# Kernel optimization log

Hardware: AMD Instinct MI355X
Metric: run time of the kernel (lower is better)

Reference implementation:

```python
import jax, jax.numpy as jnp
import numpy as np

EPS = 1e-5  # BatchNorm eps (torch default)

def _bn(x, gamma, beta):
    # training-mode BatchNorm over the edge/node (leading) axis, biased var
    mean = x.mean(axis=0, keepdims=True)
    var = x.var(axis=0, keepdims=True)
    return (x - mean) * jax.lax.rsqrt(var + EPS) * gamma + beta

def _silu(x):
    return x * jax.nn.sigmoid(x)

def setup_inputs() -> dict:
    N, E, H, NH = 50000, 800000, 128, 4
    HD = H // NH
    key = jax.random.key(0)
    ks = jax.random.split(key, 8)
    x = jax.random.normal(ks[0], (N, H), dtype=jnp.float32)
    weight = jax.random.uniform(ks[1], (N, 1), dtype=jnp.float32)  # positive fraction weights
    src = jax.random.randint(ks[2], (E,), 0, N)
    dst = jax.random.randint(ks[3], (E,), 0, N)
    # f: Linear(2H, 1) + BN(1)
    Wf = jax.random.normal(ks[4], (2 * H, 1), dtype=jnp.float32) * 0.05
    bf = jnp.zeros((1,), jnp.float32)
    f_gamma = jnp.ones((1,), jnp.float32)
    f_beta = jnp.zeros((1,), jnp.float32)
    # g: NH heads of Linear(2H, HD) + BN(HD), stacked on leading head axis
    Wg = jax.random.normal(ks[5], (NH, 2 * H, HD), dtype=jnp.float32) * 0.05
    bg = jnp.zeros((NH, HD), jnp.float32)
    g_gamma = jnp.ones((NH, HD), jnp.float32)
    g_beta = jnp.zeros((NH, HD), jnp.float32)
    # bn_nodes: BN(H)
    n_gamma = jnp.ones((H,), jnp.float32)
    n_beta = jnp.zeros((H,), jnp.float32)
    return dict(x=x, weight=weight, src=src, dst=dst, Wf=Wf, bf=bf,
                f_gamma=f_gamma, f_beta=f_beta, Wg=Wg, bg=bg,
                g_gamma=g_gamma, g_beta=g_beta, n_gamma=n_gamma, n_beta=n_beta)

def reference(x, weight, src, dst, Wf, bf, f_gamma, f_beta, Wg, bg, g_gamma, g_beta, n_gamma, n_beta):
    N = x.shape[0]
    E = src.shape[0]
    # per-edge concat of src/dst node features: [E, 2H]
    hihj = jnp.concatenate([x[src], x[dst]], axis=-1)
    # attention logit f(hihj) = SiLU(BN(Linear)) then exp: [E, 1]
    exp_e = jnp.exp(_silu(_bn(hihj @ Wf + bf, f_gamma, f_beta)))
    # weighted softmax-like normalization over incoming edges of each dst node
    we = weight[src] * exp_e                                   # [E, 1]
    sum_w_exp = jax.ops.segment_sum(we, dst, num_segments=N)   # [N, 1]
    a = we / sum_w_exp[dst]                                    # [E, 1]
    # multi-head message: a_ij * SiLU(BN(Linear_h(hihj))) per head, concat
    z = jnp.einsum('ed,hdk->ehk', hihj, Wg) + bg               # [E, NH, HD]
    z = _silu(_bn(z, g_gamma, g_beta))
    msg = (a[:, :, None] * z).reshape(E, -1)                   # [E, H]
    h = jax.ops.segment_sum(msg, dst, num_segments=N)          # [N, H]
    out = _bn(h, n_gamma, n_beta) + x                          # residual
    return out
```

## Files before the change

### kernel.cpp

```cpp
#include <hip/hip_runtime.h>
#include <hip/hip_bf16.h>
#include <math.h>

#define HDIM 128
#define PAD 64
typedef unsigned short ushort_t;
typedef unsigned int uint_t;
typedef __attribute__((ext_vector_type(8))) short bf16x8;
typedef __attribute__((ext_vector_type(4))) float f32x4;
typedef __attribute__((ext_vector_type(2))) float v2f;

__device__ __forceinline__ float wave_allreduce(float v){
  #pragma unroll
  for (int o = 1; o < 64; o <<= 1) v += __shfl_xor(v, o);
  return v;
}

__device__ __forceinline__ ushort_t f2bf(float f){
  uint_t u = __float_as_uint(f);
  uint_t r = (u + 0x7fffu + ((u >> 16) & 1u)) >> 16;
  return (ushort_t)r;
}

__device__ __forceinline__ v2f bf2(uint_t u){
  v2f r;
  r.x = __uint_as_float(u << 16);
  r.y = __uint_as_float(u & 0xffff0000u);
  return r;
}

__global__ __launch_bounds__(128) void k_wpack(const float* __restrict__ Wg,
    const float* __restrict__ Wf, ushort_t* __restrict__ W3,
    int* __restrict__ cnt, int C){
  int b = blockIdx.x;
  int k = threadIdx.x;
  if (b < 272){
    float val;
    if (b < 128)       val = Wg[(size_t)(b >> 5) * 8192 + k * 32 + (b & 31)];
    else if (b < 256){ int c2 = b - 128;
                       val = Wg[(size_t)(c2 >> 5) * 8192 + (k + 128) * 32 + (c2 & 31)]; }
    else if (b == 256) val = Wf[k];
    else if (b == 257) val = Wf[128 + k];
    else               val = 0.f;
    int idx = (((b >> 4) * 4 + (k >> 5)) * 16 + (b & 15)) * 32 + (k & 31);
    W3[idx] = f2bf(val);
  } else {
    int i = (b - 272) * 128 + k;
    if (i < C) cnt[i] = 0;
  }
}

__global__ __launch_bounds__(256) void k_gemmfill(const float* __restrict__ x,
    const ushort_t* __restrict__ W3, const float* __restrict__ weight,
    ushort_t* __restrict__ Pb, ushort_t* __restrict__ Qb,
    float* __restrict__ v, float2* __restrict__ uw2,
    const int* __restrict__ src, const int* __restrict__ dst,
    int* __restrict__ cnt, int* __restrict__ es,
    int N, int E, int FB){
  __shared__ ushort_t xl[32 * 128];
  __shared__ ushort_t cl[32 * 264];
  if ((int)blockIdx.x < FB){
    int t = blockIdx.x * 256 + threadIdx.x;
    int e0 = t * 8;
#define FILL1(d, s) { \
    int c = atomicAdd(&cnt[d], 1); \
    if (c < PAD) es[(size_t)(d) * PAD + c] = (s); }
    if (e0 + 8 <= E){
      int4 da = *(const int4*)(dst + e0);
      int4 db = *(const int4*)(dst + e0 + 4);
      int4 sa = *(const int4*)(src + e0);
      int4 sb = *(const int4*)(src + e0 + 4);
      FILL1(da.x, sa.x) FILL1(da.y, sa.y) FILL1(da.z, sa.z) FILL1(da.w, sa.w)
      FILL1(db.x, sb.x) FILL1(db.y, sb.y) FILL1(db.z, sb.z) FILL1(db.w, sb.w)
    } else {
      for (int e = e0; e < E; ++e){
        int d = dst[e];
        FILL1(d, src[e])
      }
    }
#undef FILL1
  } else {
    int tid = threadIdx.x;
    int n_base = ((int)blockIdx.x - FB) * 32;
    #pragma unroll
    for (int i = 0; i < 4; ++i){
      int cidx = i * 256 + tid;
      int row = cidx >> 5, ch = cidx & 31;
      int rowc = n_base + row; rowc = rowc < N ? rowc : N - 1;
      float4 a = *(const float4*)(x + (size_t)rowc * HDIM + ch * 4);
      uint_t lo = (uint_t)f2bf(a.x) | ((uint_t)f2bf(a.y) << 16);
      uint_t hi = (uint_t)f2bf(a.z) | ((uint_t)f2bf(a.w) << 16);
      int bo = (row * 256 + ch * 8) ^ ((row & 7) << 4);
      *(uint2*)((char*)xl + bo) = make_uint2(lo, hi);
    }
    __syncthreads();
    int wid = __builtin_amdgcn_readfirstlane(tid >> 6);
    int lane = tid & 63;
    int quad = lane >> 4, col = lane & 15;
    int strip = wid >> 1;
    int half = wid & 1;
    int tbeg = half * 8;
    int ntile = half ? 9 : 8;
    f32x4 acc[9];
    #pragma unroll
    for (int t = 0; t < 9; ++t) acc[t] = (f32x4){0.f, 0.f, 0.f, 0.f};
    int arow = strip * 16 + col;
    #pragma unroll
    for (int kk = 0; kk < 4; ++kk){
      int abyte = (arow * 256 + kk * 64 + quad * 16) ^ ((col & 7) << 4);
      bf16x8 af = *(const bf16x8*)((char*)xl + abyte);
      const ushort_t* wb = W3 + (size_t)(tbeg * 4 + kk) * 512 + col * 32 + quad * 8;
      #pragma unroll
      for (int t = 0; t < 9; ++t){
        if (t < ntile){
          bf16x8 bfr = *(const bf16x8*)(wb + (size_t)t * 2048);
          acc[t] = __builtin_amdgcn_mfma_f32_16x16x32_bf16(af, bfr, acc[t], 0, 0, 0);
        }
      }
    }
    #pragma unroll
    for (int t = 0; t < 8; ++t){
      int ct = tbeg + t;
      #pragma unroll
      for (int r = 0; r < 4; ++r){
        int lr = strip * 16 + quad * 4 + r;
        cl[lr * 264 + ct * 16 + col] = f2bf(acc[t][r]);
      }
    }
    if (half){
      #pragma unroll
      for (int r = 0; r < 4; ++r){
        int n = n_base + strip * 16 + quad * 4 + r;
        if (n < N){
          float val = acc[8][r];
          if (col == 0)      uw2[n] = make_float2(val, weight[n]);
          else if (col == 1) v[n] = val;
        }
      }
    }
    __syncthreads();
    int row = tid >> 3, seg = tid & 7;
    int n = n_base + row;
    if (n < N){
      const ushort_t* s = cl + row * 264 + seg * 32;
      uint4 w0 = *(const uint4*)(s);
      uint4 w1 = *(const uint4*)(s + 8);
      uint4 w2 = *(const uint4*)(s + 16);
      uint4 w3v = *(const uint4*)(s + 24);
      if (seg < 4){
        ushort_t* dp = Pb + (size_t)n * HDIM + seg * 32;
        *(uint4*)(dp) = w0; *(uint4*)(dp + 8) = w1;
        *(uint4*)(dp + 16) = w2; *(uint4*)(dp + 24) = w3v;
      } else {
        ushort_t* dp = Qb + (size_t)n * HDIM + (seg - 4) * 32;
        *(uint4*)(dp) = w0; *(uint4*)(dp + 8) = w1;
        *(uint4*)(dp + 16) = w2; *(uint4*)(dp + 24) = w3v;
      }
    }
  }
}

#define SH8(sjv,jj,S) \
  int S##0=__shfl(sjv,(jj)),   S##1=__shfl(sjv,(jj)+1), S##2=__shfl(sjv,(jj)+2), S##3=__shfl(sjv,(jj)+3), \
      S##4=__shfl(sjv,(jj)+4), S##5=__shfl(sjv,(jj)+5), S##6=__shfl(sjv,(jj)+6), S##7=__shfl(sjv,(jj)+7);
#define LD8(S,P) \
  uint_t P##0=Pu[(size_t)S##0*64+lane], P##1=Pu[(size_t)S##1*64+lane], \
         P##2=Pu[(size_t)S##2*64+lane], P##3=Pu[(size_t)S##3*64+lane], \
         P##4=Pu[(size_t)S##4*64+lane], P##5=Pu[(size_t)S##5*64+lane], \
         P##6=Pu[(size_t)S##6*64+lane], P##7=Pu[(size_t)S##7*64+lane];
#define SH4(sjv,jj,S) \
  int S##0=__shfl(sjv,(jj)),   S##1=__shfl(sjv,(jj)+1), S##2=__shfl(sjv,(jj)+2), S##3=__shfl(sjv,(jj)+3);
#define LD4(S,P) \
  uint_t P##0=Pu[(size_t)S##0*64+lane], P##1=Pu[(size_t)S##1*64+lane], \
         P##2=Pu[(size_t)S##2*64+lane], P##3=Pu[(size_t)S##3*64+lane];

__global__ __launch_bounds__(256) void k_gstats(const ushort_t* __restrict__ Pb,
    const ushort_t* __restrict__ Qb, const float* __restrict__ v,
    const float2* __restrict__ uw2, const int* __restrict__ es,
    const int* __restrict__ cnt, float* __restrict__ pstatG, int N){
  int lane = threadIdx.x & 63;
  int wid = __builtin_amdgcn_readfirstlane(threadIdx.x >> 6);
  int part = (int)blockIdx.x & 7;
  int Npp = (N + 7) >> 3;
  int lo = part * Npp;
  int hi = lo + Npp; if (hi > N) hi = N;
  int stp = (gridDim.x >> 3) << 2;
  const uint_t* Pu = (const uint_t*)Pb;
  const uint_t* Qu = (const uint_t*)Qb;
  v2f gs = {0.f,0.f}, gq = {0.f,0.f};
  float fs = 0.f, fq = 0.f;
  int n0 = lo + ((blockIdx.x >> 3) << 2) + wid;
  int n1 = n0 + stp;
  int dnA=0,sjA=0; uint_t qAu=0; float vA=0.f;
  int dnB=0,sjB=0; uint_t qBu=0; float vB=0.f;
  if (n0 < hi){ dnA=cnt[n0]; sjA=es[(size_t)n0*PAD+lane];
                qAu=Qu[(size_t)n0*64+lane]; vA=v[n0]; }
  if (n1 < hi){ dnB=cnt[n1]; sjB=es[(size_t)n1*PAD+lane];
                qBu=Qu[(size_t)n1*64+lane]; vB=v[n1]; }
#define GST(p,Sv,Qv) { v2f y=bf2(p); Sv+=y; Qv.x=fmaf(y.x,y.x,Qv.x); Qv.y=fmaf(y.y,y.y,Qv.y); }
#define GED8(P,Sv,Qv) GST(P##0,Sv,Qv) GST(P##1,Sv,Qv) GST(P##2,Sv,Qv) GST(P##3,Sv,Qv) \
                      GST(P##4,Sv,Qv) GST(P##5,Sv,Qv) GST(P##6,Sv,Qv) GST(P##7,Sv,Qv)
#define GED4(P,Sv,Qv) GST(P##0,Sv,Qv) GST(P##1,Sv,Qv) GST(P##2,Sv,Qv) GST(P##3,Sv,Qv)
  while (n0 < hi){
    int m0 = n0 + 2*stp, m1 = n1 + 2*stp;
    int dnC=0,sjC=0; uint_t qCu=0; float vC=0.f;
    int dnD=0,sjD=0; uint_t qDu=0; float vD=0.f;
    if (m0 < hi){ dnC=cnt[m0]; sjC=es[(size_t)m0*PAD+lane];
                  qCu=Qu[(size_t)m0*64+lane]; vC=v[m0]; }
    if (m1 < hi){ dnD=cnt[m1]; sjD=es[(size_t)m1*PAD+lane];
                  qDu=Qu[(size_t)m1*64+lane]; vD=v[m1]; }
    int dA = dnA < PAD ? dnA : PAD;
    int dB = (n1 < hi) ? (dnB < PAD ? dnB : PAD) : 0;
    if (lane < dA){ float2 uw = uw2[sjA]; float t = uw.x + vA; fs += t; fq = fmaf(t,t,fq); }
    if (lane < dB){ float2 uw = uw2[sjB]; float t = uw.x + vB; fs += t; fq = fmaf(t,t,fq); }
    v2f qa = bf2(qAu), qb = bf2(qBu);
    v2f SnA={0.f,0.f}, SSA={0.f,0.f}, SnB={0.f,0.f}, SSB={0.f,0.f};
    int j0 = 0, j1 = 0;
    for (; j0 + 7 < dA && j1 + 7 < dB; j0 += 8, j1 += 8){
      SH8(sjA,j0,xa) SH8(sjB,j1,xb)
      LD8(xa,pa) LD8(xb,pb)
      GED8(pa,SnA,SSA) GED8(pb,SnB,SSB)
    }
    for (; j0 + 7 < dA; j0 += 8){ SH8(sjA,j0,xa) LD8(xa,pa) GED8(pa,SnA,SSA) }
    for (; j0 + 3 < dA; j0 += 4){ SH4(sjA,j0,xa) LD4(xa,pa) GED4(pa,SnA,SSA) }
    for (; j0 < dA; ++j0){ int s0=__shfl(sjA,j0); uint_t p0=Pu[(size_t)s0*64+lane]; GST(p0,SnA,SSA) }
    for (; j1 + 7 < dB; j1 += 8){ SH8(sjB,j1,xb) LD8(xb,pb) GED8(pb,SnB,SSB) }
    for (; j1 + 3 < dB; j1 += 4){ SH4(sjB,j1,xb) LD4(xb,pb) GED4(pb,SnB,SSB) }
    for (; j1 < dB; ++j1){ int s0=__shfl(sjB,j1); uint_t p0=Pu[(size_t)s0*64+lane]; GST(p0,SnB,SSB) }
    float dAf = (float)dA, dBf = (float)dB;
    gs.x += SnA.x + SnB.x + dAf*qa.x + dBf*qb.x;
    gs.y += SnA.y + SnB.y + dAf*qa.y + dBf*qb.y;
    gq.x += SSA.x + SSB.x + qa.x*fmaf(dAf,qa.x,2.f*SnA.x) + qb.x*fmaf(dBf,qb.x,2.f*SnB.x);
    gq.y += SSA.y + SSB.y + qa.y*fmaf(dAf,qa.y,2.f*SnA.y) + qb.y*fmaf(dBf,qb.y,2.f*SnB.y);
    n0 = m0; n1 = m1;
    dnA=dnC; sjA=sjC; qAu=qCu; vA=vC;
    dnB=dnD; sjB=sjD; qBu=qDu; vB=vD;
  }
#undef GST
#undef GED8
#undef GED4
  fs = wave_allreduce(fs); fq = wave_allreduce(fq);
  __shared__ float red[4][258];
  red[wid][2*lane]       = gs.x; red[wid][2*lane+1]   = gs.y;
  red[wid][128+2*lane]   = gq.x; red[wid][129+2*lane] = gq.y;
  if (lane == 0){ red[wid][256] = fs; red[wid][257] = fq; }
  __syncthreads();
  for (int c = threadIdx.x; c < 258; c += 256)
    pstatG[(size_t)blockIdx.x * 258 + c] = red[0][c] + red[1][c] + red[2][c] + red[3][c];
}

__global__ __launch_bounds__(256) void k_redfin1(const float* __restrict__ pstatG,
    int NB, const float* __restrict__ g_gamma, const float* __restrict__ g_beta,
    const float* __restrict__ f_gamma, const float* __restrict__ f_beta,
    float* __restrict__ fin, long long E){
  int j = blockIdx.x;
  int c1 = (j < 128) ? j : 256;
  int c2 = (j < 128) ? 128 + j : 257;
  double s1 = 0, s2 = 0;
  for (int b = threadIdx.x; b < NB; b += 256){
    const float* pb = pstatG + (size_t)b * 258;
    s1 += (double)pb[c1]; s2 += (double)pb[c2];
  }
  __shared__ double m1[256], m2[256];
  m1[threadIdx.x] = s1; m2[threadIdx.x] = s2;
  __syncthreads();
  for (int o = 128; o; o >>= 1){
    if (threadIdx.x < o){ m1[threadIdx.x] += m1[threadIdx.x + o];
                          m2[threadIdx.x] += m2[threadIdx.x + o]; }
    __syncthreads();
  }
  if (threadIdx.x == 0){
    double m = m1[0] / (double)E;
    double var = m2[0] / (double)E - m * m;
    if (j < 128){
      float sc = (float)((double)g_gamma[j] / sqrt(var + 1e-5));
      fin[2 + j] = sc; fin[130 + j] = g_beta[j] - (float)m * sc;
    } else {
      float sc = (float)((double)f_gamma[0] / sqrt(var + 1e-5));
      fin[0] = sc; fin[1] = f_beta[0] - (float)m * sc;
    }
  }
}

__global__ __launch_bounds__(256) void k_msg(const ushort_t* __restrict__ Pb,
    const ushort_t* __restrict__ Qb, const float* __restrict__ v,
    const float2* __restrict__ uw2, const int* __restrict__ es,
    const int* __restrict__ cnt, const float* __restrict__ fin,
    float* __restrict__ h, float* __restrict__ pstatH, int N){
  int lane = threadIdx.x & 63;
  int wid = __builtin_amdgcn_readfirstlane(threadIdx.x >> 6);
  int part = (int)blockIdx.x & 7;
  int Npp = (N + 7) >> 3;
  int lo = part * Npp;
  int hi = lo + Npp; if (hi > N) hi = N;
  int stp = (gridDim.x >> 3) << 2;
  const uint_t* Pu = (const uint_t*)Pb;
  const uint_t* Qu = (const uint_t*)Qb;
  float fsc = fin[0], fsh = fin[1];
  v2f gsc = {fin[2 + 2*lane], fin[3 + 2*lane]};
  v2f gsh = {fin[130 + 2*lane], fin[131 + 2*lane]};
  v2f hs = {0.f,0.f}, hq = {0.f,0.f};
  int n0 = lo + ((blockIdx.x >> 3) << 2) + wid;
  int n1 = n0 + stp;
  int dnA=0,sjA=0; uint_t qAu=0; float vA=0.f;
  int dnB=0,sjB=0; uint_t qBu=0; float vB=0.f;
  if (n0 < hi){ dnA=cnt[n0]; sjA=es[(size_t)n0*PAD+lane];
                qAu=Qu[(size_t)n0*64+lane]; vA=v[n0]; }
  if (n1 < hi){ dnB=cnt[n1]; sjB=es[(size_t)n1*PAD+lane];
                qBu=Qu[(size_t)n1*64+lane]; vB=v[n1]; }
#define EDGE(p,a,qv,av) { v2f y = (bf2(p) + qv) * gsc + gsh; \
      float e0 = __expf(-y.x), e1 = __expf(-y.y); \
      float d0 = 1.f + e0, d1 = 1.f + e1; \
      float r = __builtin_amdgcn_rcpf(d0 * d1) * (a); \
      av.x = fmaf(y.x * d1, r, av.x); av.y = fmaf(y.y * d0, r, av.y); }
#define ASH8(wjv,jj,A) \
  float A##0=__shfl(wjv,(jj)),   A##1=__shfl(wjv,(jj)+1), A##2=__shfl(wjv,(jj)+2), A##3=__shfl(wjv,(jj)+3), \
        A##4=__shfl(wjv,(jj)+4), A##5=__shfl(wjv,(jj)+5), A##6=__shfl(wjv,(jj)+6), A##7=__shfl(wjv,(jj)+7);
#define ASH4(wjv,jj,A) \
  float A##0=__shfl(wjv,(jj)),   A##1=__shfl(wjv,(jj)+1), A##2=__shfl(wjv,(jj)+2), A##3=__shfl(wjv,(jj)+3);
#define MED8(P,A,qv,av) EDGE(P##0,A##0,qv,av) EDGE(P##1,A##1,qv,av) EDGE(P##2,A##2,qv,av) EDGE(P##3,A##3,qv,av) \
                        EDGE(P##4,A##4,qv,av) EDGE(P##5,A##5,qv,av) EDGE(P##6,A##6,qv,av) EDGE(P##7,A##7,qv,av)
#define MED4(P,A,qv,av) EDGE(P##0,A##0,qv,av) EDGE(P##1,A##1,qv,av) EDGE(P##2,A##2,qv,av) EDGE(P##3,A##3,qv,av)
  while (n0 < hi){
    int m0 = n0 + 2*stp, m1 = n1 + 2*stp;
    int dnC=0,sjC=0; uint_t qCu=0; float vC=0.f;
    int dnD=0,sjD=0; uint_t qDu=0; float vD=0.f;
    if (m0 < hi){ dnC=cnt[m0]; sjC=es[(size_t)m0*PAD+lane];
                  qCu=Qu[(size_t)m0*64+lane]; vC=v[m0]; }
    if (m1 < hi){ dnD=cnt[m1]; sjD=es[(size_t)m1*PAD+lane];
                  qDu=Qu[(size_t)m1*64+lane]; vD=v[m1]; }
    int dA = dnA < PAD ? dnA : PAD;
    int dB = (n1 < hi) ? (dnB < PAD ? dnB : PAD) : 0;
    float wjA = 0.f, wjB = 0.f;
    if (lane < dA){ float2 uw = uw2[sjA];
      float tt = fmaf(uw.x + vA, fsc, fsh);
      float sl = tt * __builtin_amdgcn_rcpf(1.f + __expf(-tt));
      wjA = uw.y * __expf(sl); }
    if (lane < dB){ float2 uw = uw2[sjB];
      float tt = fmaf(uw.x + vB, fsc, fsh);
      float sl = tt * __builtin_amdgcn_rcpf(1.f + __expf(-tt));
      wjB = uw.y * __expf(sl); }
    v2f qa = bf2(qAu), qb = bf2(qBu);
    v2f accA = {0.f,0.f}, accB = {0.f,0.f};
    int j0 = 0, j1 = 0;
    for (; j0 + 7 < dA && j1 + 7 < dB; j0 += 8, j1 += 8){
      SH8(sjA,j0,xa) SH8(sjB,j1,xb)
      ASH8(wjA,j0,aa) ASH8(wjB,j1,ab)
      LD8(xa,pa) LD8(xb,pb)
      MED8(pa,aa,qa,accA) MED8(pb,ab,qb,accB)
    }
    for (; j0 + 7 < dA; j0 += 8){ SH8(sjA,j0,xa) ASH8(wjA,j0,aa) LD8(xa,pa) MED8(pa,aa,qa,accA) }
    for (; j0 + 3 < dA; j0 += 4){ SH4(sjA,j0,xa) ASH4(wjA,j0,aa) LD4(xa,pa) MED4(pa,aa,qa,accA) }
    for (; j0 < dA; ++j0){ int s0=__shfl(sjA,j0); float a0=__shfl(wjA,j0);
                           uint_t p0=Pu[(size_t)s0*64+lane]; EDGE(p0,a0,qa,accA) }
    for (; j1 + 7 < dB; j1 += 8){ SH8(sjB,j1,xb) ASH8(wjB,j1,ab) LD8(xb,pb) MED8(pb,ab,qb,accB) }
    for (; j1 + 3 < dB; j1 += 4){ SH4(sjB,j1,xb) ASH4(wjB,j1,ab) LD4(xb,pb) MED4(pb,ab,qb,accB) }
    for (; j1 < dB; ++j1){ int s0=__shfl(sjB,j1); float a0=__shfl(wjB,j1);
                           uint_t p0=Pu[(size_t)s0*64+lane]; EDGE(p0,a0,qb,accB) }
    float swA = wjA, swB = wjB;
    #pragma unroll
    for (int o = 1; o < 64; o <<= 1){ swA += __shfl_xor(swA, o); swB += __shfl_xor(swB, o); }
    float rsA = (dA > 0) ? (1.f / swA) : 0.f;
    float rsB = (dB > 0) ? (1.f / swB) : 0.f;
    accA.x *= rsA; accA.y *= rsA;
    accB.x *= rsB; accB.y *= rsB;
    *(float2*)&h[(size_t)n0 * 128 + 2*lane] = make_float2(accA.x, accA.y);
    hs += accA; hq += accA * accA;
    if (n1 < hi){
      *(float2*)&h[(size_t)n1 * 128 + 2*lane] = make_float2(accB.x, accB.y);
      hs += accB; hq += accB * accB;
    }
    n0 = m0; n1 = m1;
    dnA=dnC; sjA=sjC; qAu=qCu; vA=vC;
    dnB=dnD; sjB=sjD; qBu=qDu; vB=vD;
  }
#undef EDGE
#undef ASH8
#undef ASH4
#undef MED8
#undef MED4
  __shared__ float red[4][256];
  red[wid][2*lane]       = hs.x; red[wid][2*lane+1]   = hs.y;
  red[wid][128+2*lane]   = hq.x; red[wid][129+2*lane] = hq.y;
  __syncthreads();
  int c = threadIdx.x;
  pstatH[(size_t)blockIdx.x * 256 + c] = red[0][c] + red[1][c] + red[2][c] + red[3][c];
}

__global__ __launch_bounds__(256) void k_redfin2(const float* __restrict__ pstatH,
    int NB, const float* __restrict__ n_gamma, const float* __restrict__ n_beta,
    float* __restrict__ fin, int N){
  int j = blockIdx.x;
  double s1 = 0, s2 = 0;
  for (int b = threadIdx.x; b < NB; b += 256){
    const float* pb = pstatH + (size_t)b * 256;
    s1 += (double)pb[j]; s2 += (double)pb[128 + j];
  }
  __shared__ double m1[256], m2[256];
  m1[threadIdx.x] = s1; m2[threadIdx.x] = s2;
  __syncthreads();
  for (int o = 128; o; o >>= 1){
    if (threadIdx.x < o){ m1[threadIdx.x] += m1[threadIdx.x + o];
                          m2[threadIdx.x] += m2[threadIdx.x + o]; }
    __syncthreads();
  }
  if (threadIdx.x == 0){
    double m = m1[0] / (double)N;
    double var = m2[0] / (double)N - m * m;
    float sc = (float)((double)n_gamma[j] / sqrt(var + 1e-5));
    fin[258 + j] = sc; fin[386 + j] = n_beta[j] - (float)m * sc;
  }
}

__global__ __launch_bounds__(256) void k_out(const float* __restrict__ h,
    const float* __restrict__ x, const float* __restrict__ fin,
    float* __restrict__ out, int total4){
  int i = blockIdx.x * 256 + threadIdx.x;
  if (i >= total4) return;
  const float4* h4 = (const float4*)h; const float4* x4 = (const float4*)x;
  float4 hv = h4[i], xv = x4[i];
  int c = (i * 4) & 127;
  float4 o;
  o.x = fmaf(hv.x, fin[258 + c],     fin[386 + c])     + xv.x;
  o.y = fmaf(hv.y, fin[258 + c + 1], fin[386 + c + 1]) + xv.y;
  o.z = fmaf(hv.z, fin[258 + c + 2], fin[386 + c + 2]) + xv.z;
  o.w = fmaf(hv.w, fin[258 + c + 3], fin[386 + c + 3]) + xv.w;
  ((float4*)out)[i] = o;
}

extern "C" void kernel_launch(void* const* d_in, const int* in_sizes, int n_in,
                              void* d_out, int out_size, void* d_ws, size_t ws_size,
                              hipStream_t stream){
  const float* x       = (const float*)d_in[0];
  const float* weight  = (const float*)d_in[1];
  const int*   src     = (const int*)d_in[2];
  const int*   dst     = (const int*)d_in[3];
  const float* Wf      = (const float*)d_in[4];
  const float* f_gamma = (const float*)d_in[6];
  const float* f_beta  = (const float*)d_in[7];
  const float* Wg      = (const float*)d_in[8];
  const float* g_gamma = (const float*)d_in[10];
  const float* g_beta  = (const float*)d_in[11];
  const float* n_gamma = (const float*)d_in[12];
  const float* n_beta  = (const float*)d_in[13];
  float* out = (float*)d_out;

  int N = in_sizes[0] / HDIM;
  int E = in_sizes[2];

  char* ws = (char*)d_ws;
  size_t off = 0;
  auto alloc = [&](size_t bytes)->char*{
    char* p = ws + off; off = (off + bytes + 255) & ~(size_t)255; return p;
  };
  ushort_t* Pb    = (ushort_t*)alloc((size_t)N * HDIM * 2);
  ushort_t* Qb    = (ushort_t*)alloc((size_t)N * HDIM * 2);
  float* h        = (float*)alloc((size_t)N * HDIM * 4);
  float* v        = (float*)alloc((size_t)N * 4);
  float2* uw2     = (float2*)alloc((size_t)N * 8);
  int* es         = (int*)alloc((size_t)N * PAD * 4);
  ushort_t* W3    = (ushort_t*)alloc((size_t)272 * 128 * 2);
  int* cnt        = (int*)alloc((size_t)N * 4);
  const int NWB = 512;
  const int NB  = NWB;
  float*  pstatG = (float*)alloc((size_t)NB * 258 * 4);
  float*  pstatH = (float*)alloc((size_t)NB * 256 * 4);
  float*  fin    = (float*)alloc(514 * 4);

  int GB = (N + 31) / 32;
  int FB = (E + 2047) / 2048;

  k_wpack   <<<272 + (N + 127) / 128, 128, 0, stream>>>(Wg, Wf, W3, cnt, N);
  k_gemmfill<<<FB + GB, 256, 0, stream>>>(x, W3, weight, Pb, Qb, v, uw2,
                                          src, dst, cnt, es, N, E, FB);
  k_gstats  <<<NWB, 256, 0, stream>>>(Pb, Qb, v, uw2, es, cnt, pstatG, N);
  k_redfin1 <<<129, 256, 0, stream>>>(pstatG, NB, g_gamma, g_beta, f_gamma, f_beta, fin, (long long)E);
  k_msg     <<<NWB, 256, 0, stream>>>(Pb, Qb, v, uw2, es, cnt, fin, h, pstatH, N);
  k_redfin2 <<<128, 256, 0, stream>>>(pstatH, NB, n_gamma, n_beta, fin, N);
  k_out     <<<(N * HDIM / 4 + 255) / 256, 256, 0, stream>>>(h, x, fin, out, N * HDIM / 4);
}
```

Before: 303.1 us.

## Split wavefronts into half-waves that gather two edges per load with 8-byte vectors

```diff
diff --git a/kernel.cpp b/kernel.cpp
--- a/kernel.cpp
+++ b/kernel.cpp
@@ -160,93 +160,127 @@
   }
 }
 
-#define SH8(sjv,jj,S) \
-  int S##0=__shfl(sjv,(jj)),   S##1=__shfl(sjv,(jj)+1), S##2=__shfl(sjv,(jj)+2), S##3=__shfl(sjv,(jj)+3), \
-      S##4=__shfl(sjv,(jj)+4), S##5=__shfl(sjv,(jj)+5), S##6=__shfl(sjv,(jj)+6), S##7=__shfl(sjv,(jj)+7);
-#define LD8(S,P) \
-  uint_t P##0=Pu[(size_t)S##0*64+lane], P##1=Pu[(size_t)S##1*64+lane], \
-         P##2=Pu[(size_t)S##2*64+lane], P##3=Pu[(size_t)S##3*64+lane], \
-         P##4=Pu[(size_t)S##4*64+lane], P##5=Pu[(size_t)S##5*64+lane], \
-         P##6=Pu[(size_t)S##6*64+lane], P##7=Pu[(size_t)S##7*64+lane];
-#define SH4(sjv,jj,S) \
-  int S##0=__shfl(sjv,(jj)),   S##1=__shfl(sjv,(jj)+1), S##2=__shfl(sjv,(jj)+2), S##3=__shfl(sjv,(jj)+3);
-#define LD4(S,P) \
-  uint_t P##0=Pu[(size_t)S##0*64+lane], P##1=Pu[(size_t)S##1*64+lane], \
-         P##2=Pu[(size_t)S##2*64+lane], P##3=Pu[(size_t)S##3*64+lane];
 
 __global__ __launch_bounds__(256) void k_gstats(const ushort_t* __restrict__ Pb,
     const ushort_t* __restrict__ Qb, const float* __restrict__ v,
     const float2* __restrict__ uw2, const int* __restrict__ es,
     const int* __restrict__ cnt, float* __restrict__ pstatG, int N){
   int lane = threadIdx.x & 63;
+  int half = lane >> 5, sl = lane & 31;
   int wid = __builtin_amdgcn_readfirstlane(threadIdx.x >> 6);
   int part = (int)blockIdx.x & 7;
   int Npp = (N + 7) >> 3;
   int lo = part * Npp;
   int hi = lo + Npp; if (hi > N) hi = N;
   int stp = (gridDim.x >> 3) << 2;
-  const uint_t* Pu = (const uint_t*)Pb;
-  const uint_t* Qu = (const uint_t*)Qb;
-  v2f gs = {0.f,0.f}, gq = {0.f,0.f};
+  const uint2* Pu2 = (const uint2*)Pb;
+  const uint2* Qu2 = (const uint2*)Qb;
+  v2f gs0={0.f,0.f}, gs1={0.f,0.f}, gq0={0.f,0.f}, gq1={0.f,0.f};
   float fs = 0.f, fq = 0.f;
   int n0 = lo + ((blockIdx.x >> 3) << 2) + wid;
   int n1 = n0 + stp;
-  int dnA=0,sjA=0; uint_t qAu=0; float vA=0.f;
-  int dnB=0,sjB=0; uint_t qBu=0; float vB=0.f;
+  int dnA=0,sjA=0; uint2 qA2=make_uint2(0,0); float vA=0.f;
+  int dnB=0,sjB=0; uint2 qB2=make_uint2(0,0); float vB=0.f;
   if (n0 < hi){ dnA=cnt[n0]; sjA=es[(size_t)n0*PAD+lane];
-                qAu=Qu[(size_t)n0*64+lane]; vA=v[n0]; }
+                qA2=Qu2[(size_t)n0*32+sl]; vA=v[n0]; }
   if (n1 < hi){ dnB=cnt[n1]; sjB=es[(size_t)n1*PAD+lane];
-                qBu=Qu[(size_t)n1*64+lane]; vB=v[n1]; }
-#define GST(p,Sv,Qv) { v2f y=bf2(p); Sv+=y; Qv.x=fmaf(y.x,y.x,Qv.x); Qv.y=fmaf(y.y,y.y,Qv.y); }
-#define GED8(P,Sv,Qv) GST(P##0,Sv,Qv) GST(P##1,Sv,Qv) GST(P##2,Sv,Qv) GST(P##3,Sv,Qv) \
-                      GST(P##4,Sv,Qv) GST(P##5,Sv,Qv) GST(P##6,Sv,Qv) GST(P##7,Sv,Qv)
-#define GED4(P,Sv,Qv) GST(P##0,Sv,Qv) GST(P##1,Sv,Qv) GST(P##2,Sv,Qv) GST(P##3,Sv,Qv)
+                qB2=Qu2[(size_t)n1*32+sl]; vB=v[n1]; }
+#define GST2(pu,S0,S1,Q0,Q1) { \
+    v2f y0=bf2(pu.x); S0+=y0; Q0.x=fmaf(y0.x,y0.x,Q0.x); Q0.y=fmaf(y0.y,y0.y,Q0.y); \
+    v2f y1=bf2(pu.y); S1+=y1; Q1.x=fmaf(y1.x,y1.x,Q1.x); Q1.y=fmaf(y1.y,y1.y,Q1.y); }
   while (n0 < hi){
     int m0 = n0 + 2*stp, m1 = n1 + 2*stp;
-    int dnC=0,sjC=0; uint_t qCu=0; float vC=0.f;
-    int dnD=0,sjD=0; uint_t qDu=0; float vD=0.f;
+    int dnC=0,sjC=0; uint2 qC2=make_uint2(0,0); float vC=0.f;
+    int dnD=0,sjD=0; uint2 qD2=make_uint2(0,0); float vD=0.f;
     if (m0 < hi){ dnC=cnt[m0]; sjC=es[(size_t)m0*PAD+lane];
-                  qCu=Qu[(size_t)m0*64+lane]; vC=v[m0]; }
+                  qC2=Qu2[(size_t)m0*32+sl]; vC=v[m0]; }
     if (m1 < hi){ dnD=cnt[m1]; sjD=es[(size_t)m1*PAD+lane];
-                  qDu=Qu[(size_t)m1*64+lane]; vD=v[m1]; }
+                  qD2=Qu2[(size_t)m1*32+sl]; vD=v[m1]; }
     int dA = dnA < PAD ? dnA : PAD;
     int dB = (n1 < hi) ? (dnB < PAD ? dnB : PAD) : 0;
     if (lane < dA){ float2 uw = uw2[sjA]; float t = uw.x + vA; fs += t; fq = fmaf(t,t,fq); }
     if (lane < dB){ float2 uw = uw2[sjB]; float t = uw.x + vB; fs += t; fq = fmaf(t,t,fq); }
-    v2f qa = bf2(qAu), qb = bf2(qBu);
-    v2f SnA={0.f,0.f}, SSA={0.f,0.f}, SnB={0.f,0.f}, SSB={0.f,0.f};
-    int j0 = 0, j1 = 0;
-    for (; j0 + 7 < dA && j1 + 7 < dB; j0 += 8, j1 += 8){
-      SH8(sjA,j0,xa) SH8(sjB,j1,xb)
-      LD8(xa,pa) LD8(xb,pb)
-      GED8(pa,SnA,SSA) GED8(pb,SnB,SSB)
-    }
-    for (; j0 + 7 < dA; j0 += 8){ SH8(sjA,j0,xa) LD8(xa,pa) GED8(pa,SnA,SSA) }
-    for (; j0 + 3 < dA; j0 += 4){ SH4(sjA,j0,xa) LD4(xa,pa) GED4(pa,SnA,SSA) }
-    for (; j0 < dA; ++j0){ int s0=__shfl(sjA,j0); uint_t p0=Pu[(size_t)s0*64+lane]; GST(p0,SnA,SSA) }
-    for (; j1 + 7 < dB; j1 += 8){ SH8(sjB,j1,xb) LD8(xb,pb) GED8(pb,SnB,SSB) }
-    for (; j1 + 3 < dB; j1 += 4){ SH4(sjB,j1,xb) LD4(xb,pb) GED4(pb,SnB,SSB) }
-    for (; j1 < dB; ++j1){ int s0=__shfl(sjB,j1); uint_t p0=Pu[(size_t)s0*64+lane]; GST(p0,SnB,SSB) }
-    float dAf = (float)dA, dBf = (float)dB;
-    gs.x += SnA.x + SnB.x + dAf*qa.x + dBf*qb.x;
-    gs.y += SnA.y + SnB.y + dAf*qa.y + dBf*qb.y;
-    gq.x += SSA.x + SSB.x + qa.x*fmaf(dAf,qa.x,2.f*SnA.x) + qb.x*fmaf(dBf,qb.x,2.f*SnB.x);
-    gq.y += SSA.y + SSB.y + qa.y*fmaf(dAf,qa.y,2.f*SnA.y) + qb.y*fmaf(dBf,qb.y,2.f*SnB.y);
+    v2f qa0=bf2(qA2.x), qa1=bf2(qA2.y), qb0=bf2(qB2.x), qb1=bf2(qB2.y);
+    v2f SA0={0.f,0.f},SA1={0.f,0.f},QA0={0.f,0.f},QA1={0.f,0.f};
+    v2f SB0={0.f,0.f},SB1={0.f,0.f},QB0={0.f,0.f},QB1={0.f,0.f};
+    int npA = dA >> 1, npB = dB >> 1;
+    int k0 = 0, k1 = 0;
+    for (; k0 + 3 < npA && k1 + 3 < npB; k0 += 4, k1 += 4){
+      int sa0=__shfl(sjA,2*k0+half),   sa1=__shfl(sjA,2*k0+2+half);
+      int sa2=__shfl(sjA,2*k0+4+half), sa3=__shfl(sjA,2*k0+6+half);
+      int sb0=__shfl(sjB,2*k1+half),   sb1=__shfl(sjB,2*k1+2+half);
+      int sb2=__shfl(sjB,2*k1+4+half), sb3=__shfl(sjB,2*k1+6+half);
+      uint2 pa0=Pu2[(size_t)sa0*32+sl], pa1=Pu2[(size_t)sa1*32+sl];
+      uint2 pa2=Pu2[(size_t)sa2*32+sl], pa3=Pu2[(size_t)sa3*32+sl];
+      uint2 pb0=Pu2[(size_t)sb0*32+sl], pb1=Pu2[(size_t)sb1*32+sl];
+      uint2 pb2=Pu2[(size_t)sb2*32+sl], pb3=Pu2[(size_t)sb3*32+sl];
+      GST2(pa0,SA0,SA1,QA0,QA1) GST2(pa1,SA0,SA1,QA0,QA1)
+      GST2(pa2,SA0,SA1,QA0,QA1) GST2(pa3,SA0,SA1,QA0,QA1)
+      GST2(pb0,SB0,SB1,QB0,QB1) GST2(pb1,SB0,SB1,QB0,QB1)
+      GST2(pb2,SB0,SB1,QB0,QB1) GST2(pb3,SB0,SB1,QB0,QB1)
+    }
+    for (; k0 + 3 < npA; k0 += 4){
+      int sa0=__shfl(sjA,2*k0+half),   sa1=__shfl(sjA,2*k0+2+half);
+      int sa2=__shfl(sjA,2*k0+4+half), sa3=__shfl(sjA,2*k0+6+half);
+      uint2 pa0=Pu2[(size_t)sa0*32+sl], pa1=Pu2[(size_t)sa1*32+sl];
+      uint2 pa2=Pu2[(size_t)sa2*32+sl], pa3=Pu2[(size_t)sa3*32+sl];
+      GST2(pa0,SA0,SA1,QA0,QA1) GST2(pa1,SA0,SA1,QA0,QA1)
+      GST2(pa2,SA0,SA1,QA0,QA1) GST2(pa3,SA0,SA1,QA0,QA1)
+    }
+    for (; k0 < npA; ++k0){
+      int s=__shfl(sjA,2*k0+half);
+      uint2 p=Pu2[(size_t)s*32+sl];
+      GST2(p,SA0,SA1,QA0,QA1)
+    }
+    if (dA & 1){
+      int s=__shfl(sjA,dA-1);
+      if (!half){ uint2 p=Pu2[(size_t)s*32+sl]; GST2(p,SA0,SA1,QA0,QA1) }
+    }
+    for (; k1 + 3 < npB; k1 += 4){
+      int sb0=__shfl(sjB,2*k1+half),   sb1=__shfl(sjB,2*k1+2+half);
+      int sb2=__shfl(sjB,2*k1+4+half), sb3=__shfl(sjB,2*k1+6+half);
+      uint2 pb0=Pu2[(size_t)sb0*32+sl], pb1=Pu2[(size_t)sb1*32+sl];
+      uint2 pb2=Pu2[(size_t)sb2*32+sl], pb3=Pu2[(size_t)sb3*32+sl];
+      GST2(pb0,SB0,SB1,QB0,QB1) GST2(pb1,SB0,SB1,QB0,QB1)
+      GST2(pb2,SB0,SB1,QB0,QB1) GST2(pb3,SB0,SB1,QB0,QB1)
+    }
+    for (; k1 < npB; ++k1){
+      int s=__shfl(sjB,2*k1+half);
+      uint2 p=Pu2[(size_t)s*32+sl];
+      GST2(p,SB0,SB1,QB0,QB1)
+    }
+    if (dB & 1){
+      int s=__shfl(sjB,dB-1);
+      if (!half){ uint2 p=Pu2[(size_t)s*32+sl]; GST2(p,SB0,SB1,QB0,QB1) }
+    }
+    float dHA = (float)((dA + 1 - half) >> 1);
+    float dHB = (float)((dB + 1 - half) >> 1);
+    gs0.x += SA0.x + dHA*qa0.x + SB0.x + dHB*qb0.x;
+    gs0.y += SA0.y + dHA*qa0.y + SB0.y + dHB*qb0.y;
+    gs1.x += SA1.x + dHA*qa1.x + SB1.x + dHB*qb1.x;
+    gs1.y += SA1.y + dHA*qa1.y + SB1.y + dHB*qb1.y;
+    gq0.x += QA0.x + qa0.x*fmaf(dHA,qa0.x,2.f*SA0.x) + QB0.x + qb0.x*fmaf(dHB,qb0.x,2.f*SB0.x);
+    gq0.y += QA0.y + qa0.y*fmaf(dHA,qa0.y,2.f*SA0.y) + QB0.y + qb0.y*fmaf(dHB,qb0.y,2.f*SB0.y);
+    gq1.x += QA1.x + qa1.x*fmaf(dHA,qa1.x,2.f*SA1.x) + QB1.x + qb1.x*fmaf(dHB,qb1.x,2.f*SB1.x);
+    gq1.y += QA1.y + qa1.y*fmaf(dHA,qa1.y,2.f*SA1.y) + QB1.y + qb1.y*fmaf(dHB,qb1.y,2.f*SB1.y);
     n0 = m0; n1 = m1;
-    dnA=dnC; sjA=sjC; qAu=qCu; vA=vC;
-    dnB=dnD; sjB=sjD; qBu=qDu; vB=vD;
-  }
-#undef GST
-#undef GED8
-#undef GED4
+    dnA=dnC; sjA=sjC; qA2=qC2; vA=vC;
+    dnB=dnD; sjB=sjD; qB2=qD2; vB=vD;
+  }
+#undef GST2
   fs = wave_allreduce(fs); fq = wave_allreduce(fq);
-  __shared__ float red[4][258];
-  red[wid][2*lane]       = gs.x; red[wid][2*lane+1]   = gs.y;
-  red[wid][128+2*lane]   = gq.x; red[wid][129+2*lane] = gq.y;
-  if (lane == 0){ red[wid][256] = fs; red[wid][257] = fq; }
+  __shared__ float red[4][2][258];
+  red[wid][half][4*sl+0] = gs0.x; red[wid][half][4*sl+1] = gs0.y;
+  red[wid][half][4*sl+2] = gs1.x; red[wid][half][4*sl+3] = gs1.y;
+  red[wid][half][128+4*sl+0] = gq0.x; red[wid][half][128+4*sl+1] = gq0.y;
+  red[wid][half][128+4*sl+2] = gq1.x; red[wid][half][128+4*sl+3] = gq1.y;
+  if (lane == 0){ red[wid][0][256] = fs; red[wid][0][257] = fq;
+                  red[wid][1][256] = 0.f; red[wid][1][257] = 0.f; }
   __syncthreads();
   for (int c = threadIdx.x; c < 258; c += 256)
-    pstatG[(size_t)blockIdx.x * 258 + c] = red[0][c] + red[1][c] + red[2][c] + red[3][c];
+    pstatG[(size_t)blockIdx.x * 258 + c] =
+      red[0][0][c]+red[0][1][c]+red[1][0][c]+red[1][1][c]
+    + red[2][0][c]+red[2][1][c]+red[3][0][c]+red[3][1][c];
 }
 
 __global__ __launch_bounds__(256) void k_redfin1(const float* __restrict__ pstatG,
@@ -288,100 +322,153 @@
     const int* __restrict__ cnt, const float* __restrict__ fin,
     float* __restrict__ h, float* __restrict__ pstatH, int N){
   int lane = threadIdx.x & 63;
+  int half = lane >> 5, sl = lane & 31;
   int wid = __builtin_amdgcn_readfirstlane(threadIdx.x >> 6);
   int part = (int)blockIdx.x & 7;
   int Npp = (N + 7) >> 3;
   int lo = part * Npp;
   int hi = lo + Npp; if (hi > N) hi = N;
   int stp = (gridDim.x >> 3) << 2;
-  const uint_t* Pu = (const uint_t*)Pb;
-  const uint_t* Qu = (const uint_t*)Qb;
+  const uint2* Pu2 = (const uint2*)Pb;
+  const uint2* Qu2 = (const uint2*)Qb;
   float fsc = fin[0], fsh = fin[1];
-  v2f gsc = {fin[2 + 2*lane], fin[3 + 2*lane]};
-  v2f gsh = {fin[130 + 2*lane], fin[131 + 2*lane]};
-  v2f hs = {0.f,0.f}, hq = {0.f,0.f};
+  v2f gscA = {fin[2 + 4*sl],   fin[3 + 4*sl]};
+  v2f gscB = {fin[4 + 4*sl],   fin[5 + 4*sl]};
+  v2f gshA = {fin[130 + 4*sl], fin[131 + 4*sl]};
+  v2f gshB = {fin[132 + 4*sl], fin[133 + 4*sl]};
+  v2f hs0={0.f,0.f}, hs1={0.f,0.f}, hq0={0.f,0.f}, hq1={0.f,0.f};
   int n0 = lo + ((blockIdx.x >> 3) << 2) + wid;
   int n1 = n0 + stp;
-  int dnA=0,sjA=0; uint_t qAu=0; float vA=0.f;
-  int dnB=0,sjB=0; uint_t qBu=0; float vB=0.f;
+  int dnA=0,sjA=0; uint2 qA2=make_uint2(0,0); float vA=0.f;
+  int dnB=0,sjB=0; uint2 qB2=make_uint2(0,0); float vB=0.f;
   if (n0 < hi){ dnA=cnt[n0]; sjA=es[(size_t)n0*PAD+lane];
-                qAu=Qu[(size_t)n0*64+lane]; vA=v[n0]; }
+                qA2=Qu2[(size_t)n0*32+sl]; vA=v[n0]; }
   if (n1 < hi){ dnB=cnt[n1]; sjB=es[(size_t)n1*PAD+lane];
-                qBu=Qu[(size_t)n1*64+lane]; vB=v[n1]; }
-#define EDGE(p,a,qv,av) { v2f y = (bf2(p) + qv) * gsc + gsh; \
-      float e0 = __expf(-y.x), e1 = __expf(-y.y); \
-      float d0 = 1.f + e0, d1 = 1.f + e1; \
-      float r = __builtin_amdgcn_rcpf(d0 * d1) * (a); \
-      av.x = fmaf(y.x * d1, r, av.x); av.y = fmaf(y.y * d0, r, av.y); }
-#define ASH8(wjv,jj,A) \
-  float A##0=__shfl(wjv,(jj)),   A##1=__shfl(wjv,(jj)+1), A##2=__shfl(wjv,(jj)+2), A##3=__shfl(wjv,(jj)+3), \
-        A##4=__shfl(wjv,(jj)+4), A##5=__shfl(wjv,(jj)+5), A##6=__shfl(wjv,(jj)+6), A##7=__shfl(wjv,(jj)+7);
-#define ASH4(wjv,jj,A) \
-  float A##0=__shfl(wjv,(jj)),   A##1=__shfl(wjv,(jj)+1), A##2=__shfl(wjv,(jj)+2), A##3=__shfl(wjv,(jj)+3);
-#define MED8(P,A,qv,av) EDGE(P##0,A##0,qv,av) EDGE(P##1,A##1,qv,av) EDGE(P##2,A##2,qv,av) EDGE(P##3,A##3,qv,av) \
-                        EDGE(P##4,A##4,qv,av) EDGE(P##5,A##5,qv,av) EDGE(P##6,A##6,qv,av) EDGE(P##7,A##7,qv,av)
-#define MED4(P,A,qv,av) EDGE(P##0,A##0,qv,av) EDGE(P##1,A##1,qv,av) EDGE(P##2,A##2,qv,av) EDGE(P##3,A##3,qv,av)
+                qB2=Qu2[(size_t)n1*32+sl]; vB=v[n1]; }
+#define MEDGE(pu,a,q0,q1,av0,av1) { \
+    v2f y0 = (bf2(pu.x) + q0) * gscA + gshA; \
+    v2f y1 = (bf2(pu.y) + q1) * gscB + gshB; \
+    float e0=__expf(-y0.x), e1=__expf(-y0.y), e2=__expf(-y1.x), e3=__expf(-y1.y); \
+    float d0=1.f+e0, d1=1.f+e1, d2=1.f+e2, d3=1.f+e3; \
+    float r0=__builtin_amdgcn_rcpf(d0*d1)*(a); \
+    float r1=__builtin_amdgcn_rcpf(d2*d3)*(a); \
+    av0.x=fmaf(y0.x*d1,r0,av0.x); av0.y=fmaf(y0.y*d0,r0,av0.y); \
+    av1.x=fmaf(y1.x*d3,r1,av1.x); av1.y=fmaf(y1.y*d2,r1,av1.y); }
   while (n0 < hi){
     int m0 = n0 + 2*stp, m1 = n1 + 2*stp;
-    int dnC=0,sjC=0; uint_t qCu=0; float vC=0.f;
-    int dnD=0,sjD=0; uint_t qDu=0; float vD=0.f;
+    int dnC=0,sjC=0; uint2 qC2=make_uint2(0,0); float vC=0.f;
+    int dnD=0,sjD=0; uint2 qD2=make_uint2(0,0); float vD=0.f;
     if (m0 < hi){ dnC=cnt[m0]; sjC=es[(size_t)m0*PAD+lane];
-                  qCu=Qu[(size_t)m0*64+lane]; vC=v[m0]; }
+                  qC2=Qu2[(size_t)m0*32+sl]; vC=v[m0]; }
     if (m1 < hi){ dnD=cnt[m1]; sjD=es[(size_t)m1*PAD+lane];
-                  qDu=Qu[(size_t)m1*64+lane]; vD=v[m1]; }
+                  qD2=Qu2[(size_t)m1*32+sl]; vD=v[m1]; }
     int dA = dnA < PAD ? dnA : PAD;
     int dB = (n1 < hi) ? (dnB < PAD ? dnB : PAD) : 0;
     float wjA = 0.f, wjB = 0.f;
     if (lane < dA){ float2 uw = uw2[sjA];
       float tt = fmaf(uw.x + vA, fsc, fsh);
-      float sl = tt * __builtin_amdgcn_rcpf(1.f + __expf(-tt));
-      wjA = uw.y * __expf(sl); }
+      float sli = tt * __builtin_amdgcn_rcpf(1.f + __expf(-tt));
+      wjA = uw.y * __expf(sli); }
     if (lane < dB){ float2 uw = uw2[sjB];
       float tt = fmaf(uw.x + vB, fsc, fsh);
-      float sl = tt * __builtin_amdgcn_rcpf(1.f + __expf(-tt));
-      wjB = uw.y * __expf(sl); }
-    v2f qa = bf2(qAu), qb = bf2(qBu);
-    v2f accA = {0.f,0.f}, accB = {0.f,0.f};
-    int j0 = 0, j1 = 0;
-    for (; j0 + 7 < dA && j1 + 7 < dB; j0 += 8, j1 += 8){
-      SH8(sjA,j0,xa) SH8(sjB,j1,xb)
-      ASH8(wjA,j0,aa) ASH8(wjB,j1,ab)
-      LD8(xa,pa) LD8(xb,pb)
-      MED8(pa,aa,qa,accA) MED8(pb,ab,qb,accB)
-    }
-    for (; j0 + 7 < dA; j0 += 8){ SH8(sjA,j0,xa) ASH8(wjA,j0,aa) LD8(xa,pa) MED8(pa,aa,qa,accA) }
-    for (; j0 + 3 < dA; j0 += 4){ SH4(sjA,j0,xa) ASH4(wjA,j0,aa) LD4(xa,pa) MED4(pa,aa,qa,accA) }
-    for (; j0 < dA; ++j0){ int s0=__shfl(sjA,j0); float a0=__shfl(wjA,j0);
-                           uint_t p0=Pu[(size_t)s0*64+lane]; EDGE(p0,a0,qa,accA) }
-    for (; j1 + 7 < dB; j1 += 8){ SH8(sjB,j1,xb) ASH8(wjB,j1,ab) LD8(xb,pb) MED8(pb,ab,qb,accB) }
-    for (; j1 + 3 < dB; j1 += 4){ SH4(sjB,j1,xb) ASH4(wjB,j1,ab) LD4(xb,pb) MED4(pb,ab,qb,accB) }
-    for (; j1 < dB; ++j1){ int s0=__shfl(sjB,j1); float a0=__shfl(wjB,j1);
-                           uint_t p0=Pu[(size_t)s0*64+lane]; EDGE(p0,a0,qb,accB) }
+      float sli = tt * __builtin_amdgcn_rcpf(1.f + __expf(-tt));
+      wjB = uw.y * __expf(sli); }
+    v2f qa0=bf2(qA2.x), qa1=bf2(qA2.y), qb0=bf2(qB2.x), qb1=bf2(qB2.y);
+    v2f accA0={0.f,0.f}, accA1={0.f,0.f}, accB0={0.f,0.f}, accB1={0.f,0.f};
+    int npA = dA >> 1, npB = dB >> 1;
+    int k0 = 0, k1 = 0;
+    for (; k0 + 3 < npA && k1 + 3 < npB; k0 += 4, k1 += 4){
+      int sa0=__shfl(sjA,2*k0+half),   sa1=__shfl(sjA,2*k0+2+half);
+      int sa2=__shfl(sjA,2*k0+4+half), sa3=__shfl(sjA,2*k0+6+half);
+      int sb0=__shfl(sjB,2*k1+half),   sb1=__shfl(sjB,2*k1+2+half);
+      int sb2=__shfl(sjB,2*k1+4+half), sb3=__shfl(sjB,2*k1+6+half);
+      float aa0=__shfl(wjA,2*k0+half),   aa1=__shfl(wjA,2*k0+2+half);
+      float aa2=__shfl(wjA,2*k0+4+half), aa3=__shfl(wjA,2*k0+6+half);
+      float ab0=__shfl(wjB,2*k1+half),   ab1=__shfl(wjB,2*k1+2+half);
+      float ab2=__shfl(wjB,2*k1+4+half), ab3=__shfl(wjB,2*k1+6+half);
+      uint2 pa0=Pu2[(size_t)sa0*32+sl], pa1=Pu2[(size_t)sa1*32+sl];
+      uint2 pa2=Pu2[(size_t)sa2*32+sl], pa3=Pu2[(size_t)sa3*32+sl];
+      uint2 pb0=Pu2[(size_t)sb0*32+sl], pb1=Pu2[(size_t)sb1*32+sl];
+      uint2 pb2=Pu2[(size_t)sb2*32+sl], pb3=Pu2[(size_t)sb3*32+sl];
+      MEDGE(pa0,aa0,qa0,qa1,accA0,accA1) MEDGE(pa1,aa1,qa0,qa1,accA0,accA1)
+      MEDGE(pa2,aa2,qa0,qa1,accA0,accA1) MEDGE(pa3,aa3,qa0,qa1,accA0,accA1)
+      MEDGE(pb0,ab0,qb0,qb1,accB0,accB1) MEDGE(pb1,ab1,qb0,qb1,accB0,accB1)
+      MEDGE(pb2,ab2,qb0,qb1,accB0,accB1) MEDGE(pb3,ab3,qb0,qb1,accB0,accB1)
+    }
+    for (; k0 + 3 < npA; k0 += 4){
+      int sa0=__shfl(sjA,2*k0+half),   sa1=__shfl(sjA,2*k0+2+half);
+      int sa2=__shfl(sjA,2*k0+4+half), sa3=__shfl(sjA,2*k0+6+half);
+      float aa0=__shfl(wjA,2*k0+half),   aa1=__shfl(wjA,2*k0+2+half);
+      float aa2=__shfl(wjA,2*k0+4+half), aa3=__shfl(wjA,2*k0+6+half);
+      uint2 pa0=Pu2[(size_t)sa0*32+sl], pa1=Pu2[(size_t)sa1*32+sl];
+      uint2 pa2=Pu2[(size_t)sa2*32+sl], pa3=Pu2[(size_t)sa3*32+sl];
+      MEDGE(pa0,aa0,qa0,qa1,accA0,accA1) MEDGE(pa1,aa1,qa0,qa1,accA0,accA1)
+      MEDGE(pa2,aa2,qa0,qa1,accA0,accA1) MEDGE(pa3,aa3,qa0,qa1,accA0,accA1)
+    }
+    for (; k0 < npA; ++k0){
+      int s=__shfl(sjA,2*k0+half); float a=__shfl(wjA,2*k0+half);
+      uint2 p=Pu2[(size_t)s*32+sl];
+      MEDGE(p,a,qa0,qa1,accA0,accA1)
+    }
+    if (dA & 1){
+      int s=__shfl(sjA,dA-1); float a=__shfl(wjA,dA-1);
+      if (!half){ uint2 p=Pu2[(size_t)s*32+sl]; MEDGE(p,a,qa0,qa1,accA0,accA1) }
+    }
+    for (; k1 + 3 < npB; k1 += 4){
+      int sb0=__shfl(sjB,2*k1+half),   sb1=__shfl(sjB,2*k1+2+half);
+      int sb2=__shfl(sjB,2*k1+4+half), sb3=__shfl(sjB,2*k1+6+half);
+      float ab0=__shfl(wjB,2*k1+half),   ab1=__shfl(wjB,2*k1+2+half);
+      float ab2=__shfl(wjB,2*k1+4+half), ab3=__shfl(wjB,2*k1+6+half);
+      uint2 pb0=Pu2[(size_t)sb0*32+sl], pb1=Pu2[(size_t)sb1*32+sl];
+      uint2 pb2=Pu2[(size_t)sb2*32+sl], pb3=Pu2[(size_t)sb3*32+sl];
+      MEDGE(pb0,ab0,qb0,qb1,accB0,accB1) MEDGE(pb1,ab1,qb0,qb1,accB0,accB1)
+      MEDGE(pb2,ab2,qb0,qb1,accB0,accB1) MEDGE(pb3,ab3,qb0,qb1,accB0,accB1)
+    }
+    for (; k1 < npB; ++k1){
+      int s=__shfl(sjB,2*k1+half); float a=__shfl(wjB,2*k1+half);
+      uint2 p=Pu2[(size_t)s*32+sl];
+      MEDGE(p,a,qb0,qb1,accB0,accB1)
+    }
+    if (dB & 1){
+      int s=__shfl(sjB,dB-1); float a=__shfl(wjB,dB-1);
+      if (!half){ uint2 p=Pu2[(size_t)s*32+sl]; MEDGE(p,a,qb0,qb1,accB0,accB1) }
+    }
     float swA = wjA, swB = wjB;
     #pragma unroll
     for (int o = 1; o < 64; o <<= 1){ swA += __shfl_xor(swA, o); swB += __shfl_xor(swB, o); }
     float rsA = (dA > 0) ? (1.f / swA) : 0.f;
     float rsB = (dB > 0) ? (1.f / swB) : 0.f;
-    accA.x *= rsA; accA.y *= rsA;
-    accB.x *= rsB; accB.y *= rsB;
-    *(float2*)&h[(size_t)n0 * 128 + 2*lane] = make_float2(accA.x, accA.y);
-    hs += accA; hq += accA * accA;
+    v2f cA0, cA1, cB0, cB1;
+    cA0.x = accA0.x*rsA; cA0.y = accA0.y*rsA; cA1.x = accA1.x*rsA; cA1.y = accA1.y*rsA;
+    cB0.x = accB0.x*rsB; cB0.y = accB0.y*rsB; cB1.x = accB1.x*rsB; cB1.y = accB1.y*rsB;
+    cA0.x += __shfl_xor(cA0.x,32); cA0.y += __shfl_xor(cA0.y,32);
+    cA1.x += __shfl_xor(cA1.x,32); cA1.y += __shfl_xor(cA1.y,32);
+    cB0.x += __shfl_xor(cB0.x,32); cB0.y += __shfl_xor(cB0.y,32);
+    cB1.x += __shfl_xor(cB1.x,32); cB1.y += __shfl_xor(cB1.y,32);
+    if (!half)
+      *(float4*)&h[(size_t)n0 * 128 + 4*sl] = make_float4(cA0.x, cA0.y, cA1.x, cA1.y);
+    hs0 += cA0; hs1 += cA1;
+    hq0.x = fmaf(cA0.x,cA0.x,hq0.x); hq0.y = fmaf(cA0.y,cA0.y,hq0.y);
+    hq1.x = fmaf(cA1.x,cA1.x,hq1.x); hq1.y = fmaf(cA1.y,cA1.y,hq1.y);
     if (n1 < hi){
-      *(float2*)&h[(size_t)n1 * 128 + 2*lane] = make_float2(accB.x, accB.y);
-      hs += accB; hq += accB * accB;
+      if (!half)
+        *(float4*)&h[(size_t)n1 * 128 + 4*sl] = make_float4(cB0.x, cB0.y, cB1.x, cB1.y);
+      hs0 += cB0; hs1 += cB1;
+      hq0.x = fmaf(cB0.x,cB0.x,hq0.x); hq0.y = fmaf(cB0.y,cB0.y,hq0.y);
+      hq1.x = fmaf(cB1.x,cB1.x,hq1.x); hq1.y = fmaf(cB1.y,cB1.y,hq1.y);
     }
     n0 = m0; n1 = m1;
-    dnA=dnC; sjA=sjC; qAu=qCu; vA=vC;
-    dnB=dnD; sjB=sjD; qBu=qDu; vB=vD;
-  }
-#undef EDGE
-#undef ASH8
-#undef ASH4
-#undef MED8
-#undef MED4
+    dnA=dnC; sjA=sjC; qA2=qC2; vA=vC;
+    dnB=dnD; sjB=sjD; qB2=qD2; vB=vD;
+  }
+#undef MEDGE
   __shared__ float red[4][256];
-  red[wid][2*lane]       = hs.x; red[wid][2*lane+1]   = hs.y;
-  red[wid][128+2*lane]   = hq.x; red[wid][129+2*lane] = hq.y;
+  if (!half){
+    red[wid][4*sl+0] = hs0.x; red[wid][4*sl+1] = hs0.y;
+    red[wid][4*sl+2] = hs1.x; red[wid][4*sl+3] = hs1.y;
+    red[wid][128+4*sl+0] = hq0.x; red[wid][128+4*sl+1] = hq0.y;
+    red[wid][128+4*sl+2] = hq1.x; red[wid][128+4*sl+3] = hq1.y;
+  }
   __syncthreads();
   int c = threadIdx.x;
   pstatH[(size_t)blockIdx.x * 256 + c] = red[0][c] + red[1][c] + red[2][c] + red[3][c];
@@ -461,7 +548,7 @@
   int* es         = (int*)alloc((size_t)N * PAD * 4);
   ushort_t* W3    = (ushort_t*)alloc((size_t)272 * 128 * 2);
   int* cnt        = (int*)alloc((size_t)N * 4);
-  const int NWB = 512;
+  const int NWB = 2048;
   const int NB  = NWB;
   float*  pstatG = (float*)alloc((size_t)NB * 258 * 4);
   float*  pstatH = (float*)alloc((size_t)NB * 256 * 4);
```

New measurement: 284.1 us. 1.07x faster.
